# Kernel optimization log

Hardware: AMD Instinct MI355X
Metric: run time of the kernel (lower is better)

## Reference

```python
import jax, jax.numpy as jnp
import numpy as np

B, N, C = 8, 2048, 256

def setup_inputs() -> dict:
    key = jax.random.key(0)
    ks = jax.random.split(key, 6)
    corr = jax.random.normal(ks[0], (B, N, N), dtype=jnp.float32)
    feat = jax.random.normal(ks[1], (B, N, C), dtype=jnp.float32)
    histogram = jax.random.uniform(ks[2], (B, N, 1), dtype=jnp.float32)
    mask = jax.random.normal(ks[3], (N, N), dtype=jnp.float32)
    # nn.Linear(C, C) params
    lim = 1.0 / np.sqrt(C)
    v_w = jax.random.uniform(ks[4], (C, C), minval=-lim, maxval=lim, dtype=jnp.float32)
    v_b = jax.random.uniform(ks[5], (C,), minval=-lim, maxval=lim, dtype=jnp.float32)
    return {"corr": corr, "feat": feat, "histogram": histogram, "mask": mask, "v_w": v_w, "v_b": v_b}

def reference(corr, feat, histogram, mask, v_w, v_b):
    # histogram is viewed/expanded in the original but never used downstream.
    # masked softmax over last axis: (b, n, n)
    attn = jax.nn.softmax(corr + mask[None, :, :], axis=-1)
    # v projection: y = feat @ v_w.T + v_b   (b, n, c)
    ref_feat_v = jnp.einsum("bnc,dc->bnd", feat, v_w) + v_b
    # attention output: (b, n, c)
    return jnp.einsum("bnm,bmc->bnc", attn, ref_feat_v)
```

## Files before the change

### kernel.cpp

```cpp
#include <hip/hip_runtime.h>
#include <hip/hip_fp16.h>


#define B_ 8
#define N_ 2048
#define C_ 256

typedef _Float16 half8  __attribute__((ext_vector_type(8)));
typedef _Float16 half4v __attribute__((ext_vector_type(4)));
typedef float    f32x4  __attribute__((ext_vector_type(4)));

static __device__ __forceinline__ void gload_lds16(const _Float16* g, _Float16* l) {
    __builtin_amdgcn_global_load_lds(
        (const __attribute__((address_space(1))) unsigned int*)g,
        (__attribute__((address_space(3))) unsigned int*)l,
        16, 0, 0);
}

__global__ __launch_bounds__(256) void k_convw(const float* __restrict__ w,
                                               _Float16* __restrict__ wh) {
    int i = (blockIdx.x * 256 + threadIdx.x) * 4;
    float4 v = *(const float4*)(w + i);
    half4v h = {(_Float16)v.x, (_Float16)v.y, (_Float16)v.z, (_Float16)v.w};
    *(half4v*)(wh + i) = h;
}

__global__ __launch_bounds__(256) void k_trans(const float* __restrict__ feat,
                                               _Float16* __restrict__ featF) {
    __shared__ _Float16 s[64][68];
    int blk  = blockIdx.x;
    int b    = blk >> 7;
    int tile = blk & 127;
    int n0   = (tile >> 2) << 6;
    int c0   = (tile & 3) << 6;
    int t    = threadIdx.x;

    const float* src = feat + ((size_t)(b * N_ + n0)) * C_ + c0;
#pragma unroll
    for (int i = 0; i < 4; ++i) {
        int idx = i * 256 + t;
        int row = idx >> 4;
        int c4  = (idx & 15) << 2;
        float4 v = *(const float4*)(src + (size_t)row * C_ + c4);
        half4v h = {(_Float16)v.x, (_Float16)v.y, (_Float16)v.z, (_Float16)v.w};
        *(half4v*)&s[row][c4] = h;
    }
    __syncthreads();

    int w = t >> 6, l = t & 63;
    int kk  = w & 1;
    int cb0 = (w >> 1) << 1;
#pragma unroll
    for (int cbi = 0; cbi < 2; ++cbi) {
        int cb = cb0 + cbi;
        half8 v;
#pragma unroll
        for (int j = 0; j < 8; ++j)
            v[j] = s[kk * 32 + ((l >> 4) << 3) + j][(cb << 4) + (l & 15)];
        _Float16* dst = featF +
            (((size_t)((b * 64 + (n0 >> 5) + kk) * 16 + (c0 >> 4) + cb)) * 64 + l) * 8;
        *(half8*)dst = v;
    }
}

__global__ __launch_bounds__(1024, 4) void k_attn(const float* __restrict__ corr,
                                                  const float* __restrict__ mask,
                                                  const _Float16* __restrict__ featF,
                                                  _Float16* __restrict__ T) {
    __shared__ _Float16 p_lds[2][64][72];
    __shared__ _Float16 f_lds[2][2][16][64][8];
    __shared__ float rowsum[64];

    const int rblk = blockIdx.x >> 3;
    const int b    = blockIdx.x & 7;
    const int r0   = rblk * 64;
    const int tg   = threadIdx.x;
    const int w    = tg >> 6, l = tg & 63;
    const int wr   = w >> 3, wc = w & 7;
    const int lrow = l & 15, kch = l >> 4;

    const int srow = tg >> 4;
    const int scol = (tg & 15) << 2;

    const float*    pc  = corr + ((size_t)(b * N_ + r0 + srow)) * N_ + scol;
    const float*    pm  = mask + ((size_t)(r0 + srow)) * N_ + scol;
    const _Float16* pfb = featF + (size_t)b * (64 * 16 * 512);

    float rs = 0.0f;
    f32x4 acc[2][2] = {};

    float4 cc = *(const float4*)pc;
    float4 mm = *(const float4*)pm;
    {
        float p0 = __expf(cc.x + mm.x), p1 = __expf(cc.y + mm.y),
              p2 = __expf(cc.z + mm.z), p3 = __expf(cc.w + mm.w);
        rs += (p0 + p1) + (p2 + p3);
        half4v h = {(_Float16)p0, (_Float16)p1, (_Float16)p2, (_Float16)p3};
        *(half4v*)&p_lds[0][srow][scol] = h;
    }
#pragma unroll
    for (int i = 0; i < 2; ++i) {
        int chunk = i * 16 + w;
        gload_lds16(pfb + chunk * 512 + l * 8, &f_lds[0][0][0][0][0] + chunk * 512);
    }
    __syncthreads();

    for (int t = 0; t < 32; ++t) {
        const int cur = t & 1, nxt = cur ^ 1;
        if (t < 31) {
            const _Float16* gsrc = pfb + (size_t)(t + 1) * 16384;
            _Float16* fdst = &f_lds[nxt][0][0][0][0];
#pragma unroll
            for (int i = 0; i < 2; ++i) {
                int chunk = i * 16 + w;
                gload_lds16(gsrc + chunk * 512 + l * 8, fdst + chunk * 512);
            }
            cc = *(const float4*)(pc + (t + 1) * 64);
            mm = *(const float4*)(pm + (t + 1) * 64);
        }
#pragma unroll
        for (int kk = 0; kk < 2; ++kk) {
            half8 a0 = *(const half8*)&p_lds[cur][wr * 32 + lrow][kk * 32 + kch * 8];
            half8 a1 = *(const half8*)&p_lds[cur][wr * 32 + 16 + lrow][kk * 32 + kch * 8];
            half8 b0 = *(const half8*)&f_lds[cur][kk][wc * 2][l][0];
            half8 b1 = *(const half8*)&f_lds[cur][kk][wc * 2 + 1][l][0];
            acc[0][0] = __builtin_amdgcn_mfma_f32_16x16x32_f16(a0, b0, acc[0][0], 0, 0, 0);
            acc[0][1] = __builtin_amdgcn_mfma_f32_16x16x32_f16(a0, b1, acc[0][1], 0, 0, 0);
            acc[1][0] = __builtin_amdgcn_mfma_f32_16x16x32_f16(a1, b0, acc[1][0], 0, 0, 0);
            acc[1][1] = __builtin_amdgcn_mfma_f32_16x16x32_f16(a1, b1, acc[1][1], 0, 0, 0);
        }
        if (t < 31) {
            float p0 = __expf(cc.x + mm.x), p1 = __expf(cc.y + mm.y),
                  p2 = __expf(cc.z + mm.z), p3 = __expf(cc.w + mm.w);
            rs += (p0 + p1) + (p2 + p3);
            half4v h = {(_Float16)p0, (_Float16)p1, (_Float16)p2, (_Float16)p3};
            *(half4v*)&p_lds[nxt][srow][scol] = h;
        }
        __syncthreads();
    }

    rs += __shfl_xor(rs, 1);
    rs += __shfl_xor(rs, 2);
    rs += __shfl_xor(rs, 4);
    rs += __shfl_xor(rs, 8);
    if ((l & 15) == 0) rowsum[srow] = rs;
    __syncthreads();

#pragma unroll
    for (int m = 0; m < 2; ++m) {
        float inv[4];
#pragma unroll
        for (int j = 0; j < 4; ++j)
            inv[j] = 1.0f / rowsum[wr * 32 + m * 16 + kch * 4 + j];
        _Float16* pT = T + ((size_t)(b * N_ + r0 + wr * 32 + m * 16 + kch * 4)) * C_
                         + wc * 32 + lrow;
#pragma unroll
        for (int j = 0; j < 4; ++j) {
#pragma unroll
            for (int n = 0; n < 2; ++n) {
                pT[(size_t)j * C_ + n * 16] = (_Float16)(acc[m][n][j] * inv[j]);
            }
        }
    }
}

__global__ __launch_bounds__(256, 2) void k_out(const _Float16* __restrict__ T,
                                                const _Float16* __restrict__ wh,
                                                const float* __restrict__ v_b,
                                                float* __restrict__ out) {
    const int blk = blockIdx.x;
    const int r0  = blk * 32;
    const int t   = threadIdx.x;
    const int w   = t >> 6, l = t & 63;
    const int wr  = w >> 1, wc = w & 1;
    const int lrow = l & 15, kch = l >> 4;

    const _Float16* pA = T  + ((size_t)(r0 + wr * 16 + lrow)) * C_ + kch * 8;
    const _Float16* pB = wh + ((size_t)(wc * 128 + lrow)) * C_ + kch * 8;

    f32x4 acc[8] = {};
#pragma unroll
    for (int step = 0; step < 8; step++) {
        half8 a = *(const half8*)(pA + step * 32);
#pragma unroll
        for (int q = 0; q < 8; q++) {
            half8 bf = *(const half8*)(pB + step * 32 + (size_t)q * 16 * C_);
            acc[q] = __builtin_amdgcn_mfma_f32_16x16x32_f16(a, bf, acc[q], 0, 0, 0);
        }
    }

    float* pO = out + ((size_t)(r0 + wr * 16 + kch * 4)) * C_ + wc * 128 + lrow;
#pragma unroll
    for (int q = 0; q < 8; q++) {
        float bias = v_b[wc * 128 + q * 16 + lrow];
#pragma unroll
        for (int j = 0; j < 4; j++) {
            pO[(size_t)j * C_ + q * 16] = acc[q][j] + bias;
        }
    }
}

extern "C" void kernel_launch(void* const* d_in, const int* in_sizes, int n_in,
                              void* d_out, int out_size, void* d_ws, size_t ws_size,
                              hipStream_t stream) {
    const float* corr = (const float*)d_in[0];
    const float* feat = (const float*)d_in[1];
    const float* mask = (const float*)d_in[3];
    const float* v_w  = (const float*)d_in[4];
    const float* v_b  = (const float*)d_in[5];
    float* out = (float*)d_out;

    char* ws = (char*)d_ws;
    _Float16* featF = (_Float16*)ws;
    _Float16* T     = (_Float16*)(ws + (size_t)8 * 1024 * 1024);
    _Float16* wh    = (_Float16*)(ws + (size_t)16 * 1024 * 1024);

    hipLaunchKernelGGL(k_trans, dim3(1024), dim3(256), 0, stream, feat, featF);
    hipLaunchKernelGGL(k_convw, dim3(64),   dim3(256), 0, stream, v_w, wh);
    hipLaunchKernelGGL(k_attn,  dim3(256),  dim3(1024), 0, stream, corr, mask, featF, T);
    hipLaunchKernelGGL(k_out,   dim3(512),  dim3(256), 0, stream, T, wh, v_b, out);
}
```

Before: 87.78 us.

## Triple-buffer feature tiles and prefetch two steps ahead in attention kernel

The attention kernel's feature-tile LDS buffer grows from two to three stages, and both the global-to-LDS feature loads and the corr/mask register loads are issued two iterations ahead. The full __syncthreads is replaced by a partial vmcnt wait plus a raw s_barrier, so in-flight prefetches for step t+2 are not drained at every iteration. The loop is unrolled by two to alternate the register prefetch buffers. This is meant to hide HBM latency better, at the cost of more LDS per block (which may cut occupancy) and hand-tuned waitcnt values that are fragile.

```diff
diff --git a/kernel.cpp b/kernel.cpp
--- a/kernel.cpp
+++ b/kernel.cpp
@@ -5,6 +5,7 @@
 #define B_ 8
 #define N_ 2048
 #define C_ 256
+#define FSZ 16384
 
 typedef _Float16 half8  __attribute__((ext_vector_type(8)));
 typedef _Float16 half4v __attribute__((ext_vector_type(4)));
@@ -68,7 +69,7 @@
                                                   const _Float16* __restrict__ featF,
                                                   _Float16* __restrict__ T) {
     __shared__ _Float16 p_lds[2][64][72];
-    __shared__ _Float16 f_lds[2][2][16][64][8];
+    __shared__ _Float16 f_lds[3][FSZ];
     __shared__ float rowsum[64];
 
     const int rblk = blockIdx.x >> 3;
@@ -89,55 +90,76 @@
     float rs = 0.0f;
     f32x4 acc[2][2] = {};
 
-    float4 cc = *(const float4*)pc;
-    float4 mm = *(const float4*)pm;
-    {
-        float p0 = __expf(cc.x + mm.x), p1 = __expf(cc.y + mm.y),
-              p2 = __expf(cc.z + mm.z), p3 = __expf(cc.w + mm.w);
-        rs += (p0 + p1) + (p2 + p3);
-        half4v h = {(_Float16)p0, (_Float16)p1, (_Float16)p2, (_Float16)p3};
-        *(half4v*)&p_lds[0][srow][scol] = h;
-    }
-#pragma unroll
-    for (int i = 0; i < 2; ++i) {
-        int chunk = i * 16 + w;
-        gload_lds16(pfb + chunk * 512 + l * 8, &f_lds[0][0][0][0][0] + chunk * 512);
-    }
+#define STAGE_F(TT, BUFI)                                                     \
+    {                                                                         \
+        _Float16* fdst = &f_lds[BUFI][0];                                     \
+        const _Float16* gsrc = pfb + (size_t)(TT) * FSZ;                      \
+        _Pragma("unroll")                                                     \
+        for (int i_ = 0; i_ < 2; ++i_) {                                      \
+            int ch_ = i_ * 16 + w;                                            \
+            gload_lds16(gsrc + ch_ * 512 + l * 8, fdst + ch_ * 512);          \
+        }                                                                     \
+    }
+
+#define EXPSTORE(TT, CC, MM)                                                  \
+    {                                                                         \
+        float p0 = __expf((CC).x + (MM).x), p1 = __expf((CC).y + (MM).y);     \
+        float p2 = __expf((CC).z + (MM).z), p3 = __expf((CC).w + (MM).w);     \
+        rs += (p0 + p1) + (p2 + p3);                                          \
+        half4v h = {(_Float16)p0, (_Float16)p1, (_Float16)p2, (_Float16)p3};  \
+        *(half4v*)&p_lds[(TT) & 1][srow][scol] = h;                           \
+    }
+
+    STAGE_F(0, 0);
+    STAGE_F(1, 1);
+    float4 cP = *(const float4*)pc;
+    float4 mP = *(const float4*)pm;
+    float4 cA = *(const float4*)(pc + 64);
+    float4 mA = *(const float4*)(pm + 64);
+    float4 cB, mB;
+    asm volatile("s_waitcnt vmcnt(0)" ::: "memory");
+    EXPSTORE(0, cP, mP);
     __syncthreads();
 
-    for (int t = 0; t < 32; ++t) {
-        const int cur = t & 1, nxt = cur ^ 1;
-        if (t < 31) {
-            const _Float16* gsrc = pfb + (size_t)(t + 1) * 16384;
-            _Float16* fdst = &f_lds[nxt][0][0][0][0];
-#pragma unroll
-            for (int i = 0; i < 2; ++i) {
-                int chunk = i * 16 + w;
-                gload_lds16(gsrc + chunk * 512 + l * 8, fdst + chunk * 512);
-            }
-            cc = *(const float4*)(pc + (t + 1) * 64);
-            mm = *(const float4*)(pm + (t + 1) * 64);
-        }
-#pragma unroll
-        for (int kk = 0; kk < 2; ++kk) {
-            half8 a0 = *(const half8*)&p_lds[cur][wr * 32 + lrow][kk * 32 + kch * 8];
-            half8 a1 = *(const half8*)&p_lds[cur][wr * 32 + 16 + lrow][kk * 32 + kch * 8];
-            half8 b0 = *(const half8*)&f_lds[cur][kk][wc * 2][l][0];
-            half8 b1 = *(const half8*)&f_lds[cur][kk][wc * 2 + 1][l][0];
-            acc[0][0] = __builtin_amdgcn_mfma_f32_16x16x32_f16(a0, b0, acc[0][0], 0, 0, 0);
-            acc[0][1] = __builtin_amdgcn_mfma_f32_16x16x32_f16(a0, b1, acc[0][1], 0, 0, 0);
-            acc[1][0] = __builtin_amdgcn_mfma_f32_16x16x32_f16(a1, b0, acc[1][0], 0, 0, 0);
-            acc[1][1] = __builtin_amdgcn_mfma_f32_16x16x32_f16(a1, b1, acc[1][1], 0, 0, 0);
-        }
-        if (t < 31) {
-            float p0 = __expf(cc.x + mm.x), p1 = __expf(cc.y + mm.y),
-                  p2 = __expf(cc.z + mm.z), p3 = __expf(cc.w + mm.w);
-            rs += (p0 + p1) + (p2 + p3);
-            half4v h = {(_Float16)p0, (_Float16)p1, (_Float16)p2, (_Float16)p3};
-            *(half4v*)&p_lds[nxt][srow][scol] = h;
-        }
-        __syncthreads();
-    }
+#define STEP(T_, CCON, MCON, CLD, MLD)                                        \
+    {                                                                         \
+        const int t_ = (T_);                                                  \
+        if (t_ < 30) {                                                        \
+            STAGE_F(t_ + 2, (t_ + 2) % 3);                                    \
+            CLD = *(const float4*)(pc + (t_ + 2) * 64);                       \
+            MLD = *(const float4*)(pm + (t_ + 2) * 64);                       \
+        }                                                                     \
+        {                                                                     \
+            const _Float16* fb = &f_lds[t_ % 3][0];                           \
+            const int par = t_ & 1;                                           \
+            _Pragma("unroll")                                                 \
+            for (int kk = 0; kk < 2; ++kk) {                                  \
+                half8 a0 = *(const half8*)&p_lds[par][wr * 32 + lrow][kk * 32 + kch * 8];      \
+                half8 a1 = *(const half8*)&p_lds[par][wr * 32 + 16 + lrow][kk * 32 + kch * 8]; \
+                half8 b0 = *(const half8*)(fb + ((kk * 16 + wc * 2) * 64 + l) * 8);            \
+                half8 b1 = *(const half8*)(fb + ((kk * 16 + wc * 2 + 1) * 64 + l) * 8);        \
+                acc[0][0] = __builtin_amdgcn_mfma_f32_16x16x32_f16(a0, b0, acc[0][0], 0, 0, 0);\
+                acc[0][1] = __builtin_amdgcn_mfma_f32_16x16x32_f16(a0, b1, acc[0][1], 0, 0, 0);\
+                acc[1][0] = __builtin_amdgcn_mfma_f32_16x16x32_f16(a1, b0, acc[1][0], 0, 0, 0);\
+                acc[1][1] = __builtin_amdgcn_mfma_f32_16x16x32_f16(a1, b1, acc[1][1], 0, 0, 0);\
+            }                                                                 \
+        }                                                                     \
+        if (t_ < 31) EXPSTORE(t_ + 1, CCON, MCON);                            \
+        if (t_ < 30) {                                                        \
+            asm volatile("s_waitcnt vmcnt(4) lgkmcnt(0)" ::: "memory");       \
+        } else {                                                              \
+            asm volatile("s_waitcnt vmcnt(0) lgkmcnt(0)" ::: "memory");       \
+        }                                                                     \
+        __builtin_amdgcn_s_barrier();                                         \
+    }
+
+    for (int th = 0; th < 16; ++th) {
+        STEP(2 * th,     cA, mA, cB, mB);
+        STEP(2 * th + 1, cB, mB, cA, mA);
+    }
+#undef STEP
+#undef STAGE_F
+#undef EXPSTORE
 
     rs += __shfl_xor(rs, 1);
     rs += __shfl_xor(rs, 2);
```

Result: faster. 80.78 us (-8.0%).
